# Optimization experiments

Hardware: AMD Instinct MI355X
Metric: run time of the kernel (lower is better)

Reference implementation:

```python
import jax, jax.numpy as jnp
import numpy as np

B, C_IN, C_HID, H, W = 4, 512, 512, 64, 64


def setup_inputs() -> dict:
    key = jax.random.key(0)
    ks = jax.random.split(key, 9)
    s_in = 1.0 / np.sqrt(C_IN)
    s_hid = 1.0 / np.sqrt(C_HID)
    return {
        "inp": jax.random.normal(ks[0], (B, C_IN, H, W), dtype=jnp.float32),
        "Wk": jax.random.normal(ks[1], (C_HID, C_IN), dtype=jnp.float32) * s_in,
        "bk": jax.random.normal(ks[2], (C_HID,), dtype=jnp.float32) * 0.01,
        "Wq": jax.random.normal(ks[3], (C_HID, C_IN), dtype=jnp.float32) * s_in,
        "bq": jax.random.normal(ks[4], (C_HID,), dtype=jnp.float32) * 0.01,
        "Wv": jax.random.normal(ks[5], (C_HID, C_IN), dtype=jnp.float32) * s_in,
        "bv": jax.random.normal(ks[6], (C_HID,), dtype=jnp.float32) * 0.01,
        "Wo": jax.random.normal(ks[7], (C_IN, C_HID), dtype=jnp.float32) * s_hid,
        "bo": jax.random.normal(ks[8], (C_IN,), dtype=jnp.float32) * 0.01,
    }


def reference(inp, Wk, bk, Wq, bq, Wv, bv, Wo, bo):
    b, _, h, w = inp.shape
    n = h * w

    def conv1x1(x, Wt, bias):  # 1x1 conv == per-pixel GEMM
        return jnp.einsum('bchw,oc->bohw', x, Wt) + bias[None, :, None, None]

    k = conv1x1(inp, Wk, bk).reshape(b, C_HID, n)   # [B,Ch,N]
    q = conv1x1(inp, Wq, bq).reshape(b, C_HID, n)
    v = conv1x1(inp, Wv, bv).reshape(b, C_HID, n)

    scale = 1.0 / jnp.sqrt(jnp.asarray(C_HID, dtype=jnp.float32))
    # weight[b,i,j] = <key_i, query_j> / sqrt(Ch); softmax over j (dim=2)
    scores = jnp.einsum('bci,bcj->bij', k, q) * scale  # [B,N,N]
    weight = jax.nn.softmax(scores, axis=2)
    # out[b,c,i] = sum_j weight[b,i,j] * v[b,c,j]
    out = jnp.einsum('bij,bcj->bci', weight, v).reshape(b, C_HID, h, w)
    return conv1x1(out, Wo, bo)  # [B,C_in,H,W]
```

## Files before the change

### kernel.cpp

```cpp
#include <hip/hip_runtime.h>
#include <hip/hip_bf16.h>


typedef __attribute__((ext_vector_type(4))) float f32x4;
typedef __attribute__((ext_vector_type(4))) int i32x4;
typedef _Float16 half8 __attribute__((ext_vector_type(8)));
typedef __attribute__((ext_vector_type(4))) short short4v;
typedef __attribute__((ext_vector_type(8))) signed char schar8;

#define SQRT_QS 0.2525200f

__device__ __forceinline__ unsigned short f2h(float f) {
  _Float16 h = (_Float16)f;
  return __builtin_bit_cast(unsigned short, h);
}

__device__ __forceinline__ void gll16(const void* g, void* l) {
  __builtin_amdgcn_global_load_lds((const __attribute__((address_space(1))) void*)g,
                                   (__attribute__((address_space(3))) void*)l, 16, 0, 0);
}

#define MFMA_F16(d, va, vb) \
  d = __builtin_amdgcn_mfma_f32_16x16x32_f16(va, vb, d, 0, 0, 0)
#define MFMA_I8(d, va, vb) \
  d = __builtin_amdgcn_mfma_i32_16x16x64_i8(va, vb, d, 0, 0, 0)

__device__ __forceinline__ void gemm_fat(
    const short* __restrict__ A, int lda,
    const short* __restrict__ B, int ldb,
    int nkt, char* sm, f32x4 (&acc)[8][4]) {
  const int tid = threadIdx.x, w = tid >> 6, lane = tid & 63;
  const int g = lane >> 4, l15 = lane & 15;
  const int swz = (l15 & 7) << 4;

  for (int t = 0; t < nkt; ++t) {
    __syncthreads();
#pragma unroll
    for (int reg = 0; reg < 3; ++reg) {
      const short* src = reg ? B : A;
      const int ld = reg ? ldb : lda;
      const int rbase = (reg == 2) ? 128 : 0;
#pragma unroll
      for (int pass = 0; pass < 4; ++pass) {
        int chunk = pass * 4 + w;
        int o = chunk * 1024 + lane * 16;
        int row = o >> 7;
        int cb = (o & 127) ^ ((row & 7) << 4);
        gll16((const char*)src + (size_t)(rbase + row) * (ld * 2) +
                  (size_t)t * 128 + cb,
              sm + reg * 16384 + chunk * 1024);
      }
    }
    __syncthreads();
#pragma unroll
    for (int ks = 0; ks < 2; ++ks) {
      half8 a[8], bb[4];
#pragma unroll
      for (int i = 0; i < 8; ++i)
        a[i] = *(const half8*)(sm + (i * 16 + l15) * 128 + ((ks * 64 + g * 16) ^ swz));
#pragma unroll
      for (int nf = 0; nf < 4; ++nf) {
        int r = w * 64 + nf * 16 + l15;
        bb[nf] = *(const half8*)(sm + 16384 + (r >> 7) * 16384 + (r & 127) * 128 +
                                 ((ks * 64 + g * 16) ^ swz));
      }
      __builtin_amdgcn_s_setprio(1);
#pragma unroll
      for (int i = 0; i < 8; ++i)
#pragma unroll
        for (int nf = 0; nf < 4; ++nf)
          MFMA_F16(acc[i][nf], a[i], bb[nf]);
      __builtin_amdgcn_s_setprio(0);
    }
  }
}

__device__ __forceinline__ void gemm_fat_i8(
    const signed char* __restrict__ A, int ldaB,
    const signed char* __restrict__ B, int ldbB,
    int nkt, char* sm, i32x4 (&acc)[8][4]) {
  const int tid = threadIdx.x, w = tid >> 6, lane = tid & 63;
  const int g = lane >> 4, l15 = lane & 15;
  const int swz = (l15 & 7) << 4;

  for (int t = 0; t < nkt; ++t) {
    __syncthreads();
#pragma unroll
    for (int reg = 0; reg < 3; ++reg) {
      const signed char* src = reg ? B : A;
      const int ld = reg ? ldbB : ldaB;
      const int rbase = (reg == 2) ? 128 : 0;
#pragma unroll
      for (int pass = 0; pass < 4; ++pass) {
        int chunk = pass * 4 + w;
        int o = chunk * 1024 + lane * 16;
        int row = o >> 7;
        int cb = (o & 127) ^ ((row & 7) << 4);
        gll16((const char*)src + (size_t)(rbase + row) * ld + (size_t)t * 128 + cb,
              sm + reg * 16384 + chunk * 1024);
      }
    }
    __syncthreads();
#pragma unroll
    for (int ks = 0; ks < 2; ++ks) {
      i32x4 a[8], bb[4];
#pragma unroll
      for (int i = 0; i < 8; ++i)
        a[i] = *(const i32x4*)(sm + (i * 16 + l15) * 128 + ((ks * 64 + g * 16) ^ swz));
#pragma unroll
      for (int nf = 0; nf < 4; ++nf) {
        int r = w * 64 + nf * 16 + l15;
        bb[nf] = *(const i32x4*)(sm + 16384 + (r >> 7) * 16384 + (r & 127) * 128 +
                                 ((ks * 64 + g * 16) ^ swz));
      }
      __builtin_amdgcn_s_setprio(1);
#pragma unroll
      for (int i = 0; i < 8; ++i)
#pragma unroll
        for (int nf = 0; nf < 4; ++nf)
          MFMA_I8(acc[i][nf], a[i], bb[nf]);
      __builtin_amdgcn_s_setprio(0);
    }
  }
}

__global__ __launch_bounds__(256) void cvt_w_kernel(
    const float* __restrict__ wk, const float* __restrict__ wq,
    const float* __restrict__ wv, const float* __restrict__ wo,
    short* __restrict__ o) {
  int z = blockIdx.y;
  const float* s = (z == 0) ? wk : (z == 1) ? wq : (z == 2) ? wv : wo;
  int i = blockIdx.x * 256 + threadIdx.x;
  float4 f = ((const float4*)s)[i];
  short4v v;
  v[0] = (short)f2h(f.x); v[1] = (short)f2h(f.y);
  v[2] = (short)f2h(f.z); v[3] = (short)f2h(f.w);
  if (z < 3) {
    *(short4v*)(o + z * 262144 + i * 4) = v;
  } else {
    int idx = i * 4, co = idx >> 9, cc = idx & 511;
    short* base = o + 786432 + co * 1024 + cc;
    *(short4v*)base = v;
    *(short4v*)(base + 512) = v;
  }
}

__global__ __launch_bounds__(256) void transpose_x_kernel(
    const float* __restrict__ inp, short* __restrict__ xt) {
  __shared__ float t[32][33];
  int tx = threadIdx.x, ty = threadIdx.y;
  int n0 = blockIdx.x * 32, c0 = blockIdx.y * 32, b = blockIdx.z;
  const float* src = inp + ((size_t)(b * 512 + c0)) * 4096 + n0;
#pragma unroll
  for (int r = 0; r < 4; ++r) t[ty + r * 8][tx] = src[(ty + r * 8) * 4096 + tx];
  __syncthreads();
  short* dst = xt + ((size_t)((b << 12) + n0)) * 512 + c0;
#pragma unroll
  for (int r = 0; r < 4; ++r) dst[(ty + r * 8) * 512 + tx] = (short)f2h(t[tx][ty + r * 8]);
}

__global__ __launch_bounds__(256, 2) void kqv_kernel(
    const short* __restrict__ xt,
    const short* __restrict__ wk, const short* __restrict__ wq, const short* __restrict__ wv,
    const float* __restrict__ bk, const float* __restrict__ bq, const float* __restrict__ bv,
    short* __restrict__ kth, short* __restrict__ qth,
    short* __restrict__ vc) {
  __shared__ char sm[49152];
  const int bid = blockIdx.x;
  const int xcd = bid & 7, s = bid >> 3;
  const int gg = (s / 12) * 8 + xcd;
  const int t = s % 12;
  const int z = (t < 8) ? (t >> 2) : 2;
  const short *A, *B;
  int arow0, brow0;
  if (z < 2) {
    arow0 = gg * 256 + ((t >> 1) & 1) * 128;
    brow0 = (t & 1) * 256;
    A = xt + (size_t)arow0 * 512;
    B = ((z == 0) ? wk : wq) + (size_t)brow0 * 512;
  } else {
    arow0 = (t - 8) * 128;
    brow0 = gg * 256;
    A = wv + (size_t)arow0 * 512;
    B = xt + (size_t)brow0 * 512;
  }
  f32x4 acc[8][4] = {};
  gemm_fat(A, 512, B, 512, 8, sm, acc);
  const int tid = threadIdx.x, w = tid >> 6, lane = tid & 63;
  const int gq = lane >> 4, l15 = lane & 15;
#pragma unroll
  for (int mf = 0; mf < 8; ++mf)
#pragma unroll
    for (int nf = 0; nf < 4; ++nf)
#pragma unroll
      for (int r = 0; r < 4; ++r) {
        int row = mf * 16 + gq * 4 + r;
        int col = w * 64 + nf * 16 + l15;
        float v = acc[mf][nf][r];
        if (z == 2) {
          vc[(size_t)(arow0 + row) * 16384 + brow0 + col] =
              (short)f2h(v + bv[arow0 + row]);
        } else {
          short* dst = (z == 0) ? kth : qth;
          float bias = (z == 0) ? bk[brow0 + col] : bq[brow0 + col];
          dst[(size_t)(arow0 + row) * 512 + brow0 + col] = (short)f2h(v + bias);
        }
      }
}

__global__ __launch_bounds__(256) void quant_kernel(
    const short* __restrict__ src, signed char* __restrict__ dst,
    float* __restrict__ scl) {
  const int row = blockIdx.x * 4 + (threadIdx.x >> 6);
  const int lane = threadIdx.x & 63;
  half8 v = *(const half8*)(src + (size_t)row * 512 + lane * 8);
  float f[8];
  float m = 0.f;
#pragma unroll
  for (int e = 0; e < 8; ++e) { f[e] = (float)v[e]; m = fmaxf(m, fabsf(f[e])); }
#pragma unroll
  for (int off = 1; off < 64; off <<= 1) m = fmaxf(m, __shfl_xor(m, off));
  m = fmaxf(m, 1e-6f);
  const float inv = 127.0f / m;
  schar8 q;
#pragma unroll
  for (int e = 0; e < 8; ++e) q[e] = (signed char)(int)rintf(f[e] * inv);
  *(schar8*)(dst + (size_t)row * 512 + lane * 8) = q;
  if (lane == 0) scl[row] = m * (SQRT_QS / 127.0f);
}

__global__ __launch_bounds__(256, 2) void gemm_s_kernel(
    const signed char* __restrict__ kt8, const signed char* __restrict__ qt8,
    const float* __restrict__ sk, const float* __restrict__ sq,
    short* __restrict__ P, float* __restrict__ Lpart) {
  __shared__ char sm[49152];
  const int bid = blockIdx.x;
  const int xcd = bid & 7, s = bid >> 3;
  const int b = xcd >> 1, h = xcd & 1;
  const int it = s >> 3, jt = s & 7;
  const int i0 = it * 128, jt0 = jt * 256;
  const signed char* A = kt8 + ((size_t)((b << 12) + i0)) * 512;
  const signed char* B = qt8 + ((size_t)((b << 12) + h * 2048 + jt0)) * 512;
  i32x4 acc[8][4] = {};
  gemm_fat_i8(A, 512, B, 512, 4, sm, acc);
  const int tid = threadIdx.x, w = tid >> 6, lane = tid & 63;
  const int gq = lane >> 4, l15 = lane & 15;
  const float* skp = sk + (b << 12) + i0;
  const float* sqp = sq + (b << 12) + h * 2048 + jt0;
  float sqc[4];
#pragma unroll
  for (int nf = 0; nf < 4; ++nf) sqc[nf] = sqp[w * 64 + nf * 16 + l15];
  short* Pb = P + (size_t)h * 33554432 + ((size_t)((b << 12) + i0)) * 2048 + jt0;
  float psum[8][4];
#pragma unroll
  for (int mf = 0; mf < 8; ++mf)
#pragma unroll
    for (int r = 0; r < 4; ++r) psum[mf][r] = 0.f;
#pragma unroll
  for (int mf = 0; mf < 8; ++mf) {
    float skr[4];
#pragma unroll
    for (int r = 0; r < 4; ++r) skr[r] = skp[mf * 16 + gq * 4 + r];
#pragma unroll
    for (int nf = 0; nf < 4; ++nf)
#pragma unroll
      for (int r = 0; r < 4; ++r) {
        float p = exp2f((float)acc[mf][nf][r] * skr[r] * sqc[nf] - 4.0f);
        psum[mf][r] += p;
        int row = mf * 16 + gq * 4 + r;
        int col = w * 64 + nf * 16 + l15;
        Pb[(size_t)row * 2048 + col] = (short)f2h(p);
      }
  }
  const int jp = (h * 2048 + jt0 + w * 64) >> 6;
  float* Lp = Lpart + (((size_t)b * 64 + jp) << 12) + i0;
#pragma unroll
  for (int mf = 0; mf < 8; ++mf)
#pragma unroll
    for (int r = 0; r < 4; ++r) {
      float ss = psum[mf][r];
      ss += __shfl_xor(ss, 1); ss += __shfl_xor(ss, 2);
      ss += __shfl_xor(ss, 4); ss += __shfl_xor(ss, 8);
      if (l15 == 0) Lp[mf * 16 + gq * 4 + r] = ss;
    }
}

__global__ __launch_bounds__(256, 2) void gemm_pv_kernel(
    const short* __restrict__ P, const short* __restrict__ vc,
    short* __restrict__ otab) {
  __shared__ char sm[49152];
  const int bid = blockIdx.x;
  const int xcd = bid & 7, s = bid >> 3;
  const int b = xcd >> 1, h = xcd & 1;
  const int it = s >> 1, ct = s & 1;
  const int i0 = it * 128, c0 = ct * 256;
  const short* A = P + (size_t)h * 33554432 + ((size_t)((b << 12) + i0)) * 2048;
  const short* B = vc + (size_t)c0 * 16384 + (b << 12) + h * 2048;
  f32x4 acc[8][4] = {};
  gemm_fat(A, 2048, B, 16384, 32, sm, acc);
  const int tid = threadIdx.x, w = tid >> 6, lane = tid & 63;
  const int gq = lane >> 4, l15 = lane & 15;
  short* Ob = otab + ((size_t)((b << 12) + i0)) * 1024 + h * 512 + c0;
#pragma unroll
  for (int mf = 0; mf < 8; ++mf)
#pragma unroll
    for (int nf = 0; nf < 4; ++nf)
#pragma unroll
      for (int r = 0; r < 4; ++r) {
        int row = mf * 16 + gq * 4 + r;
        int col = w * 64 + nf * 16 + l15;
        Ob[(size_t)row * 1024 + col] = (short)f2h(acc[mf][nf][r]);
      }
}

__global__ __launch_bounds__(256) void lred_kernel(
    const float* __restrict__ Lpart, float* __restrict__ linv) {
  int i = blockIdx.x * 256 + threadIdx.x;
  int b = i >> 12;
  float s = 0.f;
#pragma unroll 8
  for (int jp = 0; jp < 64; ++jp) s += Lpart[(((size_t)b * 64 + jp) << 12) + (i & 4095)];
  linv[i] = 1.0f / s;
}

__global__ __launch_bounds__(256, 2) void gemm_out_kernel(
    const short* __restrict__ wdup, const short* __restrict__ otab,
    const float* __restrict__ bo, const float* __restrict__ linv,
    float* __restrict__ out) {
  __shared__ char sm[49152];
  const int bid = blockIdx.x;
  const int xcd = bid & 7, s = bid >> 3;
  const int b = xcd >> 1, ch = xcd & 1;
  const int cot = ch * 2 + (s & 1);
  const int nt = s >> 1;
  const int arow0 = cot * 128;
  const int bn0 = nt * 256;
  const short* A = wdup + (size_t)arow0 * 1024;
  const short* B = otab + ((size_t)((b << 12) + bn0)) * 1024;
  f32x4 acc[8][4] = {};
  gemm_fat(A, 1024, B, 1024, 16, sm, acc);
  const int tid = threadIdx.x, w = tid >> 6, lane = tid & 63;
  const int gq = lane >> 4, l15 = lane & 15;
#pragma unroll
  for (int mf = 0; mf < 8; ++mf) {
    int co = arow0 + mf * 16 + gq * 4;
#pragma unroll
    for (int nf = 0; nf < 4; ++nf) {
      int nl = bn0 + w * 64 + nf * 16 + l15;
      float li = linv[(b << 12) + nl];
#pragma unroll
      for (int r = 0; r < 4; ++r)
        out[((size_t)(b * 512 + co + r) << 12) + nl] = acc[mf][nf][r] * li + bo[co + r];
    }
  }
}

extern "C" void kernel_launch(void* const* d_in, const int* in_sizes, int n_in,
                              void* d_out, int out_size, void* d_ws, size_t ws_size,
                              hipStream_t stream) {
  const float* inp = (const float*)d_in[0];
  const float* Wk = (const float*)d_in[1];
  const float* bk = (const float*)d_in[2];
  const float* Wq = (const float*)d_in[3];
  const float* bq = (const float*)d_in[4];
  const float* Wv = (const float*)d_in[5];
  const float* bv = (const float*)d_in[6];
  const float* Wo = (const float*)d_in[7];
  const float* bo = (const float*)d_in[8];
  float* out = (float*)d_out;
  char* ws = (char*)d_ws;
  const size_t MB = 1048576;
  signed char* kt8 = (signed char*)(ws);
  signed char* qt8 = (signed char*)(ws + 8 * MB);
  float* sk    = (float*)(ws + 16 * MB);
  short* vc    = (short*)(ws + 32 * MB);
  short* wb    = (short*)(ws + 48 * MB);
  short* xt    = (short*)(ws + 51 * MB);
  float* Lpart = (float*)(ws + 51 * MB);
  float* linv  = (float*)(ws + 55 * MB);
  short* P     = (short*)(ws + 67 * MB);
  short* kth   = (short*)(ws + 67 * MB);
  short* qth   = (short*)(ws + 83 * MB);
  short* otab  = (short*)(ws + 195 * MB);

  (void)in_sizes; (void)n_in; (void)out_size; (void)ws_size;

  cvt_w_kernel<<<dim3(256, 4), 256, 0, stream>>>(Wk, Wq, Wv, Wo, wb);
  transpose_x_kernel<<<dim3(128, 16, 4), dim3(32, 8, 1), 0, stream>>>(inp, xt);
  kqv_kernel<<<768, 256, 0, stream>>>(
      xt, wb, wb + 262144, wb + 524288, bk, bq, bv, kth, qth, vc);
  quant_kernel<<<8192, 256, 0, stream>>>(kth, kt8, sk);
  gemm_s_kernel<<<2048, 256, 0, stream>>>(
      kt8, qt8, sk, sk + 16384, P, Lpart);
  gemm_pv_kernel<<<512, 256, 0, stream>>>(P, vc, otab);
  lred_kernel<<<64, 256, 0, stream>>>(Lpart, linv);
  gemm_out_kernel<<<256, 256, 0, stream>>>(wb + 786432, otab, bo, linv, out);
}
```

Before: 266.8 us.

## Double-buffer LDS and enlarge GEMM tiles to 256x256 with 8 waves

Replaces the single-buffered GEMM mainloop with a double-buffered one. The next K-tile is prefetched via global_load_lds while the current one is computed, leaving one barrier per iteration instead of two. Each block now uses 512 threads arranged 2x4 over a 256x256 output tile, backed by 128KB of dynamic LDS. The aim is to overlap memory with MFMA work and raise operand reuse. The cost is half as many blocks: gemm_out launches only 128, fewer than the CU count. The large LDS footprint also limits occupancy to one block per CU.

```diff
diff --git a/kernel.cpp b/kernel.cpp
--- a/kernel.cpp
+++ b/kernel.cpp
@@ -25,45 +25,54 @@
 #define MFMA_I8(d, va, vb) \
   d = __builtin_amdgcn_mfma_i32_16x16x64_i8(va, vb, d, 0, 0, 0)
 
-__device__ __forceinline__ void gemm_fat(
+__device__ __forceinline__ void gemm_db(
     const short* __restrict__ A, int lda,
     const short* __restrict__ B, int ldb,
     int nkt, char* sm, f32x4 (&acc)[8][4]) {
   const int tid = threadIdx.x, w = tid >> 6, lane = tid & 63;
   const int g = lane >> 4, l15 = lane & 15;
+  const int wm = w >> 2, wn = w & 3;
   const int swz = (l15 & 7) << 4;
-
+  const int brow = (wn & 1) << 6;
+
+  auto stage = [&](int t, int buf) {
+    if (t >= nkt) return;
+    char* base = sm + (buf << 16);
+#pragma unroll
+    for (int c = 0; c < 4; ++c) {
+      int chunk = c * 8 + w;
+      int o = (chunk << 10) | (lane << 4);
+      int row = o >> 7, cb = (o & 127) ^ ((row & 7) << 4);
+      gll16((const char*)A + (size_t)row * (lda * 2) + (size_t)t * 128 + cb,
+            base + (chunk << 10));
+    }
+#pragma unroll
+    for (int c = 0; c < 4; ++c) {
+      int chunk = c * 8 + w;
+      int o = (chunk << 10) | (lane << 4);
+      int row = o >> 7, cb = (o & 127) ^ ((row & 7) << 4);
+      gll16((const char*)B + (size_t)row * (ldb * 2) + (size_t)t * 128 + cb,
+            base + 32768 + (chunk << 10));
+    }
+  };
+
+  stage(0, 0);
+  __syncthreads();
   for (int t = 0; t < nkt; ++t) {
-    __syncthreads();
-#pragma unroll
-    for (int reg = 0; reg < 3; ++reg) {
-      const short* src = reg ? B : A;
-      const int ld = reg ? ldb : lda;
-      const int rbase = (reg == 2) ? 128 : 0;
-#pragma unroll
-      for (int pass = 0; pass < 4; ++pass) {
-        int chunk = pass * 4 + w;
-        int o = chunk * 1024 + lane * 16;
-        int row = o >> 7;
-        int cb = (o & 127) ^ ((row & 7) << 4);
-        gll16((const char*)src + (size_t)(rbase + row) * (ld * 2) +
-                  (size_t)t * 128 + cb,
-              sm + reg * 16384 + chunk * 1024);
-      }
-    }
-    __syncthreads();
+    const int buf = t & 1;
+    stage(t + 1, buf ^ 1);
+    const char* SA = sm + (buf << 16) + (wm << 14);
+    const char* SB = sm + (buf << 16) + 32768 + ((wn >> 1) << 14);
 #pragma unroll
     for (int ks = 0; ks < 2; ++ks) {
       half8 a[8], bb[4];
 #pragma unroll
       for (int i = 0; i < 8; ++i)
-        a[i] = *(const half8*)(sm + (i * 16 + l15) * 128 + ((ks * 64 + g * 16) ^ swz));
-#pragma unroll
-      for (int nf = 0; nf < 4; ++nf) {
-        int r = w * 64 + nf * 16 + l15;
-        bb[nf] = *(const half8*)(sm + 16384 + (r >> 7) * 16384 + (r & 127) * 128 +
+        a[i] = *(const half8*)(SA + (i * 16 + l15) * 128 + ((ks * 64 + g * 16) ^ swz));
+#pragma unroll
+      for (int nf = 0; nf < 4; ++nf)
+        bb[nf] = *(const half8*)(SB + (brow + nf * 16 + l15) * 128 +
                                  ((ks * 64 + g * 16) ^ swz));
-      }
       __builtin_amdgcn_s_setprio(1);
 #pragma unroll
       for (int i = 0; i < 8; ++i)
@@ -72,47 +81,58 @@
           MFMA_F16(acc[i][nf], a[i], bb[nf]);
       __builtin_amdgcn_s_setprio(0);
     }
-  }
-}
-
-__device__ __forceinline__ void gemm_fat_i8(
+    __syncthreads();
+  }
+}
+
+__device__ __forceinline__ void gemm_db_i8(
     const signed char* __restrict__ A, int ldaB,
     const signed char* __restrict__ B, int ldbB,
     int nkt, char* sm, i32x4 (&acc)[8][4]) {
   const int tid = threadIdx.x, w = tid >> 6, lane = tid & 63;
   const int g = lane >> 4, l15 = lane & 15;
+  const int wm = w >> 2, wn = w & 3;
   const int swz = (l15 & 7) << 4;
-
+  const int brow = (wn & 1) << 6;
+
+  auto stage = [&](int t, int buf) {
+    if (t >= nkt) return;
+    char* base = sm + (buf << 16);
+#pragma unroll
+    for (int c = 0; c < 4; ++c) {
+      int chunk = c * 8 + w;
+      int o = (chunk << 10) | (lane << 4);
+      int row = o >> 7, cb = (o & 127) ^ ((row & 7) << 4);
+      gll16((const char*)A + (size_t)row * ldaB + (size_t)t * 128 + cb,
+            base + (chunk << 10));
+    }
+#pragma unroll
+    for (int c = 0; c < 4; ++c) {
+      int chunk = c * 8 + w;
+      int o = (chunk << 10) | (lane << 4);
+      int row = o >> 7, cb = (o & 127) ^ ((row & 7) << 4);
+      gll16((const char*)B + (size_t)row * ldbB + (size_t)t * 128 + cb,
+            base + 32768 + (chunk << 10));
+    }
+  };
+
+  stage(0, 0);
+  __syncthreads();
   for (int t = 0; t < nkt; ++t) {
-    __syncthreads();
-#pragma unroll
-    for (int reg = 0; reg < 3; ++reg) {
-      const signed char* src = reg ? B : A;
-      const int ld = reg ? ldbB : ldaB;
-      const int rbase = (reg == 2) ? 128 : 0;
-#pragma unroll
-      for (int pass = 0; pass < 4; ++pass) {
-        int chunk = pass * 4 + w;
-        int o = chunk * 1024 + lane * 16;
-        int row = o >> 7;
-        int cb = (o & 127) ^ ((row & 7) << 4);
-        gll16((const char*)src + (size_t)(rbase + row) * ld + (size_t)t * 128 + cb,
-              sm + reg * 16384 + chunk * 1024);
-      }
-    }
-    __syncthreads();
+    const int buf = t & 1;
+    stage(t + 1, buf ^ 1);
+    const char* SA = sm + (buf << 16) + (wm << 14);
+    const char* SB = sm + (buf << 16) + 32768 + ((wn >> 1) << 14);
 #pragma unroll
     for (int ks = 0; ks < 2; ++ks) {
       i32x4 a[8], bb[4];
 #pragma unroll
       for (int i = 0; i < 8; ++i)
-        a[i] = *(const i32x4*)(sm + (i * 16 + l15) * 128 + ((ks * 64 + g * 16) ^ swz));
-#pragma unroll
-      for (int nf = 0; nf < 4; ++nf) {
-        int r = w * 64 + nf * 16 + l15;
-        bb[nf] = *(const i32x4*)(sm + 16384 + (r >> 7) * 16384 + (r & 127) * 128 +
+        a[i] = *(const i32x4*)(SA + (i * 16 + l15) * 128 + ((ks * 64 + g * 16) ^ swz));
+#pragma unroll
+      for (int nf = 0; nf < 4; ++nf)
+        bb[nf] = *(const i32x4*)(SB + (brow + nf * 16 + l15) * 128 +
                                  ((ks * 64 + g * 16) ^ swz));
-      }
       __builtin_amdgcn_s_setprio(1);
 #pragma unroll
       for (int i = 0; i < 8; ++i)
@@ -121,6 +141,7 @@
           MFMA_I8(acc[i][nf], a[i], bb[nf]);
       __builtin_amdgcn_s_setprio(0);
     }
+    __syncthreads();
   }
 }
 
@@ -159,43 +180,44 @@
   for (int r = 0; r < 4; ++r) dst[(ty + r * 8) * 512 + tx] = (short)f2h(t[tx][ty + r * 8]);
 }
 
-__global__ __launch_bounds__(256, 2) void kqv_kernel(
+__global__ __launch_bounds__(512, 2) void kqv_kernel(
     const short* __restrict__ xt,
     const short* __restrict__ wk, const short* __restrict__ wq, const short* __restrict__ wv,
     const float* __restrict__ bk, const float* __restrict__ bq, const float* __restrict__ bv,
     short* __restrict__ kth, short* __restrict__ qth,
     short* __restrict__ vc) {
-  __shared__ char sm[49152];
+  extern __shared__ char sm[];
   const int bid = blockIdx.x;
   const int xcd = bid & 7, s = bid >> 3;
-  const int gg = (s / 12) * 8 + xcd;
-  const int t = s % 12;
-  const int z = (t < 8) ? (t >> 2) : 2;
+  const int gg = (s / 6) * 8 + xcd;
+  const int t = s % 6;
+  const int z = t >> 1;
   const short *A, *B;
   int arow0, brow0;
   if (z < 2) {
-    arow0 = gg * 256 + ((t >> 1) & 1) * 128;
+    arow0 = gg * 256;
     brow0 = (t & 1) * 256;
     A = xt + (size_t)arow0 * 512;
     B = ((z == 0) ? wk : wq) + (size_t)brow0 * 512;
   } else {
-    arow0 = (t - 8) * 128;
+    arow0 = (t - 4) * 256;
     brow0 = gg * 256;
     A = wv + (size_t)arow0 * 512;
     B = xt + (size_t)brow0 * 512;
   }
   f32x4 acc[8][4] = {};
-  gemm_fat(A, 512, B, 512, 8, sm, acc);
+  gemm_db(A, 512, B, 512, 8, sm, acc);
   const int tid = threadIdx.x, w = tid >> 6, lane = tid & 63;
   const int gq = lane >> 4, l15 = lane & 15;
+  const int wm = w >> 2, wn = w & 3;
 #pragma unroll
   for (int mf = 0; mf < 8; ++mf)
 #pragma unroll
     for (int nf = 0; nf < 4; ++nf)
 #pragma unroll
       for (int r = 0; r < 4; ++r) {
-        int row = mf * 16 + gq * 4 + r;
-        int col = w * 64 + nf * 16 + l15;
+        int row = wm * 128 + mf * 16 + gq * 4 + r;
+        int col = wn * 64 + nf * 16 + l15;
         float v = acc[mf][nf][r];
         if (z == 2) {
           vc[(size_t)(arow0 + row) * 16384 + brow0 + col] =
@@ -229,27 +251,28 @@
   if (lane == 0) scl[row] = m * (SQRT_QS / 127.0f);
 }
 
-__global__ __launch_bounds__(256, 2) void gemm_s_kernel(
+__global__ __launch_bounds__(512, 2) void gemm_s_kernel(
     const signed char* __restrict__ kt8, const signed char* __restrict__ qt8,
     const float* __restrict__ sk, const float* __restrict__ sq,
     short* __restrict__ P, float* __restrict__ Lpart) {
-  __shared__ char sm[49152];
+  extern __shared__ char sm[];
   const int bid = blockIdx.x;
   const int xcd = bid & 7, s = bid >> 3;
   const int b = xcd >> 1, h = xcd & 1;
   const int it = s >> 3, jt = s & 7;
-  const int i0 = it * 128, jt0 = jt * 256;
+  const int i0 = it * 256, jt0 = jt * 256;
   const signed char* A = kt8 + ((size_t)((b << 12) + i0)) * 512;
   const signed char* B = qt8 + ((size_t)((b << 12) + h * 2048 + jt0)) * 512;
   i32x4 acc[8][4] = {};
-  gemm_fat_i8(A, 512, B, 512, 4, sm, acc);
+  gemm_db_i8(A, 512, B, 512, 4, sm, acc);
   const int tid = threadIdx.x, w = tid >> 6, lane = tid & 63;
   const int gq = lane >> 4, l15 = lane & 15;
-  const float* skp = sk + (b << 12) + i0;
+  const int wm = w >> 2, wn = w & 3;
+  const float* skp = sk + (b << 12) + i0 + wm * 128;
   const float* sqp = sq + (b << 12) + h * 2048 + jt0;
   float sqc[4];
 #pragma unroll
-  for (int nf = 0; nf < 4; ++nf) sqc[nf] = sqp[w * 64 + nf * 16 + l15];
+  for (int nf = 0; nf < 4; ++nf) sqc[nf] = sqp[wn * 64 + nf * 16 + l15];
   short* Pb = P + (size_t)h * 33554432 + ((size_t)((b << 12) + i0)) * 2048 + jt0;
   float psum[8][4];
 #pragma unroll
@@ -267,13 +290,13 @@
       for (int r = 0; r < 4; ++r) {
         float p = exp2f((float)acc[mf][nf][r] * skr[r] * sqc[nf] - 4.0f);
         psum[mf][r] += p;
-        int row = mf * 16 + gq * 4 + r;
-        int col = w * 64 + nf * 16 + l15;
+        int row = wm * 128 + mf * 16 + gq * 4 + r;
+        int col = wn * 64 + nf * 16 + l15;
         Pb[(size_t)row * 2048 + col] = (short)f2h(p);
       }
   }
-  const int jp = (h * 2048 + jt0 + w * 64) >> 6;
-  float* Lp = Lpart + (((size_t)b * 64 + jp) << 12) + i0;
+  const int jp = (h * 2048 + jt0 + wn * 64) >> 6;
+  float* Lp = Lpart + (((size_t)b * 64 + jp) << 12) + i0 + wm * 128;
 #pragma unroll
   for (int mf = 0; mf < 8; ++mf)
 #pragma unroll
@@ -285,21 +308,22 @@
     }
 }
 
-__global__ __launch_bounds__(256, 2) void gemm_pv_kernel(
+__global__ __launch_bounds__(512, 2) void gemm_pv_kernel(
     const short* __restrict__ P, const short* __restrict__ vc,
     short* __restrict__ otab) {
-  __shared__ char sm[49152];
+  extern __shared__ char sm[];
   const int bid = blockIdx.x;
   const int xcd = bid & 7, s = bid >> 3;
   const int b = xcd >> 1, h = xcd & 1;
   const int it = s >> 1, ct = s & 1;
-  const int i0 = it * 128, c0 = ct * 256;
+  const int i0 = it * 256, c0 = ct * 256;
   const short* A = P + (size_t)h * 33554432 + ((size_t)((b << 12) + i0)) * 2048;
   const short* B = vc + (size_t)c0 * 16384 + (b << 12) + h * 2048;
   f32x4 acc[8][4] = {};
-  gemm_fat(A, 2048, B, 16384, 32, sm, acc);
+  gemm_db(A, 2048, B, 16384, 32, sm, acc);
   const int tid = threadIdx.x, w = tid >> 6, lane = tid & 63;
   const int gq = lane >> 4, l15 = lane & 15;
+  const int wm = w >> 2, wn = w & 3;
   short* Ob = otab + ((size_t)((b << 12) + i0)) * 1024 + h * 512 + c0;
 #pragma unroll
   for (int mf = 0; mf < 8; ++mf)
@@ -307,8 +331,8 @@
     for (int nf = 0; nf < 4; ++nf)
 #pragma unroll
       for (int r = 0; r < 4; ++r) {
-        int row = mf * 16 + gq * 4 + r;
-        int col = w * 64 + nf * 16 + l15;
+        int row = wm * 128 + mf * 16 + gq * 4 + r;
+        int col = wn * 64 + nf * 16 + l15;
         Ob[(size_t)row * 1024 + col] = (short)f2h(acc[mf][nf][r]);
       }
 }
@@ -323,30 +347,29 @@
   linv[i] = 1.0f / s;
 }
 
-__global__ __launch_bounds__(256, 2) void gemm_out_kernel(
+__global__ __launch_bounds__(512, 2) void gemm_out_kernel(
     const short* __restrict__ wdup, const short* __restrict__ otab,
     const float* __restrict__ bo, const float* __restrict__ linv,
     float* __restrict__ out) {
-  __shared__ char sm[49152];
+  extern __shared__ char sm[];
   const int bid = blockIdx.x;
-  const int xcd = bid & 7, s = bid >> 3;
-  const int b = xcd >> 1, ch = xcd & 1;
-  const int cot = ch * 2 + (s & 1);
-  const int nt = s >> 1;
-  const int arow0 = cot * 128;
+  const int xcd = bid & 7, nt = bid >> 3;
+  const int b = xcd >> 1, coh = xcd & 1;
+  const int arow0 = coh * 256;
   const int bn0 = nt * 256;
   const short* A = wdup + (size_t)arow0 * 1024;
   const short* B = otab + ((size_t)((b << 12) + bn0)) * 1024;
   f32x4 acc[8][4] = {};
-  gemm_fat(A, 1024, B, 1024, 16, sm, acc);
+  gemm_db(A, 1024, B, 1024, 16, sm, acc);
   const int tid = threadIdx.x, w = tid >> 6, lane = tid & 63;
   const int gq = lane >> 4, l15 = lane & 15;
+  const int wm = w >> 2, wn = w & 3;
 #pragma unroll
   for (int mf = 0; mf < 8; ++mf) {
-    int co = arow0 + mf * 16 + gq * 4;
+    int co = arow0 + wm * 128 + mf * 16 + gq * 4;
 #pragma unroll
     for (int nf = 0; nf < 4; ++nf) {
-      int nl = bn0 + w * 64 + nf * 16 + l15;
+      int nl = bn0 + wn * 64 + nf * 16 + l15;
       float li = linv[(b << 12) + nl];
 #pragma unroll
       for (int r = 0; r < 4; ++r)
@@ -385,14 +408,23 @@
 
   (void)in_sizes; (void)n_in; (void)out_size; (void)ws_size;
 
+  hipFuncSetAttribute((const void*)kqv_kernel,
+                      hipFuncAttributeMaxDynamicSharedMemorySize, 131072);
+  hipFuncSetAttribute((const void*)gemm_s_kernel,
+                      hipFuncAttributeMaxDynamicSharedMemorySize, 131072);
+  hipFuncSetAttribute((const void*)gemm_pv_kernel,
+                      hipFuncAttributeMaxDynamicSharedMemorySize, 131072);
+  hipFuncSetAttribute((const void*)gemm_out_kernel,
+                      hipFuncAttributeMaxDynamicSharedMemorySize, 131072);
+
   cvt_w_kernel<<<dim3(256, 4), 256, 0, stream>>>(Wk, Wq, Wv, Wo, wb);
   transpose_x_kernel<<<dim3(128, 16, 4), dim3(32, 8, 1), 0, stream>>>(inp, xt);
-  kqv_kernel<<<768, 256, 0, stream>>>(
+  kqv_kernel<<<384, 512, 131072, stream>>>(
       xt, wb, wb + 262144, wb + 524288, bk, bq, bv, kth, qth, vc);
   quant_kernel<<<8192, 256, 0, stream>>>(kth, kt8, sk);
-  gemm_s_kernel<<<2048, 256, 0, stream>>>(
+  gemm_s_kernel<<<1024, 512, 131072, stream>>>(
       kt8, qt8, sk, sk + 16384, P, Lpart);
-  gemm_pv_kernel<<<512, 256, 0, stream>>>(P, vc, otab);
+  gemm_pv_kernel<<<256, 512, 131072, stream>>>(P, vc, otab);
   lred_kernel<<<64, 256, 0, stream>>>(Lpart, linv);
-  gemm_out_kernel<<<256, 256, 0, stream>>>(wb + 786432, otab, bo, linv, out);
-}
+  gemm_out_kernel<<<128, 512, 131072, stream>>>(wb + 786432, otab, bo, linv, out);
+}
```

Measured after the change: 272.6 us. +2.2%, slower.
